# Kernel tuning notes

Hardware: AMD Instinct MI355X
Metric: run time of the kernel (lower is better)

## Reference

```python
import jax, jax.numpy as jnp
import numpy as np

B, N, E = 1, 100000, 1250000
IN, OUT = 128, 64


def setup_inputs() -> dict:
    key = jax.random.key(0)
    k = jax.random.split(key, 5)
    x = jax.random.normal(k[0], (B, N, IN), jnp.float32)
    edge_index = jax.random.randint(k[1], (B, 2, E), 0, N, dtype=jnp.int32)
    rank_mapping = jnp.zeros((2, E), jnp.int32)  # single-rank: all zeros
    W1 = jax.random.normal(k[2], (IN, OUT), jnp.float32) / np.sqrt(IN)
    Wp = jax.random.normal(k[3], (2 * OUT, 1), jnp.float32) / np.sqrt(2 * OUT)
    bp = jnp.zeros((1,), jnp.float32)
    bias = jnp.zeros((OUT,), jnp.float32)
    return {"x": x, "edge_index": edge_index, "rank_mapping": rank_mapping,
            "W1": W1, "Wp": Wp, "bp": bp, "bias": bias}


def reference(x, edge_index, rank_mapping, W1, Wp, bp, bias):
    # x: [B, N, IN]; edge_index: [B, 2, E]
    del rank_mapping  # comm routing metadata; identity on a single rank
    n = x.shape[1]
    h = jnp.einsum('bnf,fo->bno', x, W1)          # conv1 (no bias)
    src = edge_index[:, 0, :]                     # [B, E]
    dst = edge_index[:, 1, :]
    h_i = jnp.take_along_axis(h, dst[..., None], axis=1)   # gather at dst
    h_j = jnp.take_along_axis(h, src[..., None], axis=1)   # gather at src
    messages = jnp.concatenate([h_i, h_j], axis=-1)        # [B, E, 2*OUT]
    s = jnp.einsum('bec,co->beo', messages, Wp) + bp       # project_message
    s = jnp.where(s >= 0, s, 0.2 * s)                      # LeakyReLU(0.2)
    numerator = jnp.exp(s)                                 # [B, E, 1]
    seg = jax.vmap(lambda v, i: jax.ops.segment_sum(v, i, num_segments=n))
    denominator = seg(numerator, dst)                      # [B, N, 1]
    # NOTE: original gathers denominator with the *src* indices — replicated.
    denom_e = jnp.take_along_axis(denominator, src[..., None], axis=1)
    alpha = numerator / (denom_e + 1e-16)                  # [B, E, 1]
    out = seg(h_j * alpha, dst)                            # scatter-aggregate
    return out + bias
```

## Files before the change

### kernel.cpp

```cpp
#include <hip/hip_runtime.h>


#define MAXB 1024
#define EPB 4096
#define BIN_CAP 2560

typedef __attribute__((ext_vector_type(8))) short short8v;
typedef __attribute__((ext_vector_type(4))) float floatx4;

static __device__ __forceinline__ float bf2f(unsigned short u) {
    unsigned v = (unsigned)u << 16;
    return __builtin_bit_cast(float, v);
}
static __device__ __forceinline__ unsigned short f2bf(float f) {
    unsigned u = __builtin_bit_cast(unsigned, f);
    u = (u + 0x7FFFu + ((u >> 16) & 1u)) >> 16;
    return (unsigned short)u;
}

__global__ __launch_bounds__(256) void fused_nt_count_kernel(
    const float* __restrict__ x, const float* __restrict__ W1,
    const float* __restrict__ Wp, const int* __restrict__ ei,
    unsigned short* __restrict__ hbD, float* __restrict__ aArr,
    float* __restrict__ bArr, int* __restrict__ C, int N, int E, int G8, int B)
{
    __shared__ __align__(16) unsigned short w1b[4][4][4][16][8];
    __shared__ int cnt[MAXB];
    const int tid = threadIdx.x;

    if (blockIdx.x < G8) {
        const int g = blockIdx.x;
        for (int i = tid; i < B; i += 256) cnt[i] = 0;
        __syncthreads();
        const int base = g * EPB;
        #pragma unroll
        for (int k = 0; k < EPB / 256; ++k) {
            int e = base + k * 256 + tid;
            if (e < E) atomicAdd(&cnt[ei[E + e] >> 7], 1);
        }
        __syncthreads();
        for (int i = tid; i < B; i += 256) C[(size_t)g * B + i] = cnt[i];
        return;
    }

    for (int i = tid; i < 128 * 64; i += 256) {
        int k = i >> 6, o = i & 63;
        w1b[k >> 5][o >> 4][(k >> 3) & 3][o & 15][k & 7] = f2bf(W1[i]);
    }

    const int w = tid >> 6, lane = tid & 63;
    const int hi = lane >> 4, col = lane & 15;
    float wpa4[4], wpb4[4];
    #pragma unroll
    for (int ot = 0; ot < 4; ++ot) {
        wpa4[ot] = Wp[ot * 16 + col];
        wpb4[ot] = Wp[64 + ot * 16 + col];
    }
    __syncthreads();

    const int grp0 = (blockIdx.x - G8) * 4;
    #pragma unroll
    for (int gi = 0; gi < 4; ++gi) {
        const int gbase = (grp0 + gi) * 64;
        if (gbase >= N) break;
        const int n0 = gbase + w * 16;
        int arow = n0 + col; if (arow >= N) arow = N - 1;
        const float* xrow = x + (size_t)arow * 128 + hi * 8;

        floatx4 acc[4] = {{0.f,0.f,0.f,0.f},{0.f,0.f,0.f,0.f},
                          {0.f,0.f,0.f,0.f},{0.f,0.f,0.f,0.f}};
        #pragma unroll
        for (int kb = 0; kb < 4; ++kb) {
            float4 x0 = *reinterpret_cast<const float4*>(xrow + kb * 32);
            float4 x1 = *reinterpret_cast<const float4*>(xrow + kb * 32 + 4);
            short8v af;
            af[0] = (short)f2bf(x0.x); af[1] = (short)f2bf(x0.y);
            af[2] = (short)f2bf(x0.z); af[3] = (short)f2bf(x0.w);
            af[4] = (short)f2bf(x1.x); af[5] = (short)f2bf(x1.y);
            af[6] = (short)f2bf(x1.z); af[7] = (short)f2bf(x1.w);
            #pragma unroll
            for (int ot = 0; ot < 4; ++ot) {
                short8v bf = *reinterpret_cast<const short8v*>(&w1b[kb][ot][hi][col][0]);
                acc[ot] = __builtin_amdgcn_mfma_f32_16x16x32_bf16(af, bf, acc[ot], 0, 0, 0);
            }
        }

        #pragma unroll
        for (int ot = 0; ot < 4; ++ot) {
            #pragma unroll
            for (int r = 0; r < 4; ++r) {
                int n = n0 + hi * 4 + r;
                if (n < N) hbD[(size_t)n * 64 + ot * 16 + col] = f2bf(acc[ot][r]);
            }
        }
        #pragma unroll
        for (int r = 0; r < 4; ++r) {
            float pa = acc[0][r] * wpa4[0] + acc[1][r] * wpa4[1]
                     + acc[2][r] * wpa4[2] + acc[3][r] * wpa4[3];
            float pb = acc[0][r] * wpb4[0] + acc[1][r] * wpb4[1]
                     + acc[2][r] * wpb4[2] + acc[3][r] * wpb4[3];
            #pragma unroll
            for (int m = 1; m <= 8; m <<= 1) {
                pa += __shfl_xor(pa, m);
                pb += __shfl_xor(pb, m);
            }
            int n = n0 + hi * 4 + r;
            if (col == r && n < N) { aArr[n] = pa; bArr[n] = pb; }
        }
    }
}

__global__ __launch_bounds__(256) void colscan_kernel(
    int* __restrict__ C, int* __restrict__ S, int G8, int B)
{
    __shared__ int s[256];
    const int b = blockIdx.x, t = threadIdx.x;
    const int gp = G8 >> 3;
    int i0 = 2 * t, i1 = 2 * t + 1;
    int ga = 8 * (i0 % gp) + (i0 / gp);
    int gb = 8 * (i1 % gp) + (i1 / gp);
    int c0 = (i0 < G8) ? C[(size_t)ga * B + b] : 0;
    int c1 = (i1 < G8) ? C[(size_t)gb * B + b] : 0;
    int v = c0 + c1;
    s[t] = v;
    __syncthreads();
    for (int off = 1; off < 256; off <<= 1) {
        int u = (t >= off) ? s[t - off] : 0;
        __syncthreads();
        s[t] += u;
        __syncthreads();
    }
    int ex = s[t] - v;
    if (i0 < G8) C[(size_t)ga * B + b] = ex;
    if (i1 < G8) C[(size_t)gb * B + b] = ex + c0;
    if (t == 255) S[b] = s[255];
}

__global__ __launch_bounds__(256) void binscan_kernel(
    const int* __restrict__ S, int* __restrict__ binStart,
    int* __restrict__ offsets, int B, int N, int E)
{
    __shared__ int ts[256];
    const int t = threadIdx.x;
    const int chunk = (B + 255) >> 8;
    const int base = t * chunk, lim = min(B, base + chunk);
    int s = 0;
    for (int i = base; i < lim; ++i) s += S[i];
    ts[t] = s;
    __syncthreads();
    for (int off = 1; off < 256; off <<= 1) {
        int u = (t >= off) ? ts[t - off] : 0;
        __syncthreads();
        ts[t] += u;
        __syncthreads();
    }
    int run = ts[t] - s;
    for (int i = base; i < lim; ++i) { binStart[i] = run; run += S[i]; }
    if (t == 0) { binStart[B] = E; offsets[N] = E; }
}

__global__ __launch_bounds__(1024) void pass2_kernel(
    const int* __restrict__ ei, const float* __restrict__ aArr,
    const float* __restrict__ bArr, const float* __restrict__ bp,
    const int* __restrict__ C, const int* __restrict__ binStart,
    int2* __restrict__ staging, int E, int B)
{
    __shared__ int cur[MAXB];
    const int g = blockIdx.x, t = threadIdx.x;
    for (int i = t; i < B; i += 1024)
        cur[i] = binStart[i] + C[(size_t)g * B + i];
    __syncthreads();
    const float bp0 = bp[0];
    const int base = g * EPB;
    #pragma unroll
    for (int k = 0; k < EPB / 1024; ++k) {
        int e = base + k * 1024 + t;
        if (e >= E) break;
        int src = ei[e];
        int dst = ei[E + e];
        float s = aArr[dst] + bArr[src] + bp0;
        s = (s >= 0.f) ? s : 0.2f * s;
        float num = __expf(s);
        int bin = dst >> 7;
        int pos = atomicAdd(&cur[bin], 1);
        staging[pos] = make_int2(((dst & 127) << 17) | src, __float_as_int(num));
    }
}

__global__ __launch_bounds__(256) void localsort_kernel(
    const int* __restrict__ binStart, int2* __restrict__ staging,
    int* __restrict__ offsets, float* __restrict__ invD, int N)
{
    __shared__ int2 sEnt[BIN_CAP];
    __shared__ int sCnt[256], sScan[256], sCur[128];
    __shared__ float dsum[128];
    const int b = blockIdx.x, t = threadIdx.x;
    const int sBeg = binStart[b];
    const int count = min(binStart[b + 1] - sBeg, BIN_CAP);

    sCnt[t] = 0;
    if (t < 128) { sCur[t] = 0; dsum[t] = 0.f; }
    __syncthreads();
    for (int i = t; i < count; i += 256) {
        int2 e = staging[sBeg + i];
        sEnt[i] = e;
        int dl = e.x >> 17;
        atomicAdd(&sCnt[dl], 1);
        atomicAdd(&dsum[dl], __int_as_float(e.y));
    }
    __syncthreads();
    const int n0 = b << 7;
    const int Cl = min(128, N - n0);
    if (t < Cl) invD[n0 + t] = 1.f / (dsum[t] + 1e-16f);
    int v = sCnt[t];
    sScan[t] = v;
    __syncthreads();
    for (int off = 1; off < 256; off <<= 1) {
        int u = (t >= off) ? sScan[t - off] : 0;
        __syncthreads();
        sScan[t] += u;
        __syncthreads();
    }
    int ex = sScan[t] - v;
    __syncthreads();
    sScan[t] = ex;
    if (t < Cl) offsets[n0 + t] = sBeg + ex;
    __syncthreads();
    for (int i = t; i < count; i += 256) {
        int2 e = sEnt[i];
        int dl = e.x >> 17;
        int pos = sBeg + sScan[dl] + atomicAdd(&sCur[dl], 1);
        staging[pos] = make_int2(e.x & 0x1FFFF, e.y);
    }
}

__global__ __launch_bounds__(256) void aggregate_kernel(
    const int* __restrict__ offsets, const int2* __restrict__ sortedPair,
    const uint2* __restrict__ hbQ, const float* __restrict__ invD,
    const float* __restrict__ bias, float* __restrict__ out, int N)
{
    int gw = (blockIdx.x * blockDim.x + threadIdx.x) >> 6;
    int lane = threadIdx.x & 63;
    if (gw >= N) return;
    int beg = offsets[gw], end = offsets[gw + 1];
    const int quarter = lane >> 4;
    const int cg = lane & 15;
    float a0 = 0.f, a1 = 0.f, a2 = 0.f, a3 = 0.f;
    for (int e0 = beg; e0 < end; e0 += 64) {
        int idx = e0 + lane;
        int srcL = 0; float wL = 0.f;
        if (idx < end) {
            int2 p = sortedPair[idx];
            srcL = p.x;
            wL = __int_as_float(p.y) * invD[p.x];
        }
        int cnt = min(64, end - e0);
        int j = 0;
        for (; j + 16 <= cnt; j += 16) {
            #pragma unroll
            for (int u = 0; u < 4; ++u) {
                int jj = j + 4 * u + quarter;
                int s = __shfl(srcL, jj);
                float wv = __shfl(wL, jj);
                uint2 g = hbQ[(size_t)s * 16 + cg];
                a0 = fmaf(bf2f((unsigned short)(g.x & 0xFFFFu)), wv, a0);
                a1 = fmaf(bf2f((unsigned short)(g.x >> 16)), wv, a1);
                a2 = fmaf(bf2f((unsigned short)(g.y & 0xFFFFu)), wv, a2);
                a3 = fmaf(bf2f((unsigned short)(g.y >> 16)), wv, a3);
            }
        }
        for (; j < cnt; j += 4) {
            int jj = j + quarter;
            int s = __shfl(srcL, jj);
            float wv = __shfl(wL, jj);
            uint2 g = hbQ[(size_t)s * 16 + cg];
            a0 = fmaf(bf2f((unsigned short)(g.x & 0xFFFFu)), wv, a0);
            a1 = fmaf(bf2f((unsigned short)(g.x >> 16)), wv, a1);
            a2 = fmaf(bf2f((unsigned short)(g.y & 0xFFFFu)), wv, a2);
            a3 = fmaf(bf2f((unsigned short)(g.y >> 16)), wv, a3);
        }
    }
    a0 += __shfl_xor(a0, 16); a0 += __shfl_xor(a0, 32);
    a1 += __shfl_xor(a1, 16); a1 += __shfl_xor(a1, 32);
    a2 += __shfl_xor(a2, 16); a2 += __shfl_xor(a2, 32);
    a3 += __shfl_xor(a3, 16); a3 += __shfl_xor(a3, 32);
    if (lane < 16) {
        float4 bq = reinterpret_cast<const float4*>(bias)[cg];
        float4 o;
        o.x = a0 + bq.x; o.y = a1 + bq.y; o.z = a2 + bq.z; o.w = a3 + bq.w;
        reinterpret_cast<float4*>(out)[(size_t)gw * 16 + cg] = o;
    }
}

extern "C" void kernel_launch(void* const* d_in, const int* in_sizes, int n_in,
                              void* d_out, int out_size, void* d_ws, size_t ws_size,
                              hipStream_t stream) {
    const float* x    = (const float*)d_in[0];
    const int*   ei   = (const int*)d_in[1];
    const float* W1   = (const float*)d_in[3];
    const float* Wp   = (const float*)d_in[4];
    const float* bp   = (const float*)d_in[5];
    const float* bias = (const float*)d_in[6];
    float* out = (float*)d_out;

    const int N = in_sizes[0] / 128;
    const int E = in_sizes[1] / 2;
    const int B = (N + 127) >> 7;
    const int G = (E + EPB - 1) / EPB;
    const int G8 = (G + 7) & ~7;
    const int NTB = (N + 255) / 256;

    unsigned short* hbD = (unsigned short*)d_ws;
    float* aArr     = (float*)(hbD + (size_t)N * 64);
    float* bArr     = aArr + N;
    float* invD     = bArr + N;
    int*   C        = (int*)(invD + N);
    int*   S        = C + (size_t)G8 * B;
    int*   binStart = S + B;
    int*   offsets  = binStart + (B + 1);
    int*   stRaw    = offsets + (N + 1);
    stRaw = (int*)(((uintptr_t)stRaw + 7) & ~(uintptr_t)7);
    int2*  staging  = (int2*)stRaw;

    fused_nt_count_kernel<<<G8 + NTB, 256, 0, stream>>>(
        x, W1, Wp, ei, hbD, aArr, bArr, C, N, E, G8, B);

    colscan_kernel<<<B, 256, 0, stream>>>(C, S, G8, B);

    binscan_kernel<<<1, 256, 0, stream>>>(S, binStart, offsets, B, N, E);

    pass2_kernel<<<G8, 1024, 0, stream>>>(ei, aArr, bArr, bp, C, binStart,
                                          staging, E, B);

    localsort_kernel<<<B, 256, 0, stream>>>(binStart, staging, offsets, invD, N);

    aggregate_kernel<<<(N * 64 + 255) / 256, 256, 0, stream>>>(
        offsets, staging, reinterpret_cast<const uint2*>(hbD), invD, bias, out, N);
}
```

Baseline: 118.7 us.

## Accumulate softmax denominator with global atomics and prenormalize edge weights in localsort

Moves the per-destination denominator sum out of the localsort shared-memory reduction and into global float atomics in pass2, using a zeroed denom buffer. Localsort now divides each edge's numerator by denom[src] and stores the final weight, so aggregate no longer gathers invD per edge. The cost is 1.25M global atomics plus an extra memset launch. Atomic float ordering makes the sums nondeterministic.

```diff
diff --git a/kernel.cpp b/kernel.cpp
--- a/kernel.cpp
+++ b/kernel.cpp
@@ -163,7 +163,7 @@
     const int* __restrict__ ei, const float* __restrict__ aArr,
     const float* __restrict__ bArr, const float* __restrict__ bp,
     const int* __restrict__ C, const int* __restrict__ binStart,
-    int2* __restrict__ staging, int E, int B)
+    int2* __restrict__ staging, float* __restrict__ denom, int E, int B)
 {
     __shared__ int cur[MAXB];
     const int g = blockIdx.x, t = threadIdx.x;
@@ -181,6 +181,7 @@
         float s = aArr[dst] + bArr[src] + bp0;
         s = (s >= 0.f) ? s : 0.2f * s;
         float num = __expf(s);
+        atomicAdd(&denom[dst], num);
         int bin = dst >> 7;
         int pos = atomicAdd(&cur[bin], 1);
         staging[pos] = make_int2(((dst & 127) << 17) | src, __float_as_int(num));
@@ -189,55 +190,53 @@
 
 __global__ __launch_bounds__(256) void localsort_kernel(
     const int* __restrict__ binStart, int2* __restrict__ staging,
-    int* __restrict__ offsets, float* __restrict__ invD, int N)
+    int* __restrict__ offsets, const float* __restrict__ denom, int N)
 {
     __shared__ int2 sEnt[BIN_CAP];
     __shared__ int sCnt[256], sScan[256], sCur[128];
-    __shared__ float dsum[128];
     const int b = blockIdx.x, t = threadIdx.x;
     const int sBeg = binStart[b];
     const int count = min(binStart[b + 1] - sBeg, BIN_CAP);
 
     sCnt[t] = 0;
-    if (t < 128) { sCur[t] = 0; dsum[t] = 0.f; }
+    if (t < 128) sCur[t] = 0;
     __syncthreads();
     for (int i = t; i < count; i += 256) {
         int2 e = staging[sBeg + i];
         sEnt[i] = e;
-        int dl = e.x >> 17;
-        atomicAdd(&sCnt[dl], 1);
-        atomicAdd(&dsum[dl], __int_as_float(e.y));
-    }
-    __syncthreads();
+        atomicAdd(&sCnt[e.x >> 17], 1);
+    }
+    __syncthreads();
+    int v = sCnt[t];
+    sScan[t] = v;
+    __syncthreads();
+    for (int off = 1; off < 256; off <<= 1) {
+        int u = (t >= off) ? sScan[t - off] : 0;
+        __syncthreads();
+        sScan[t] += u;
+        __syncthreads();
+    }
+    int ex = sScan[t] - v;
+    __syncthreads();
+    sScan[t] = ex;
     const int n0 = b << 7;
     const int Cl = min(128, N - n0);
-    if (t < Cl) invD[n0 + t] = 1.f / (dsum[t] + 1e-16f);
-    int v = sCnt[t];
-    sScan[t] = v;
-    __syncthreads();
-    for (int off = 1; off < 256; off <<= 1) {
-        int u = (t >= off) ? sScan[t - off] : 0;
-        __syncthreads();
-        sScan[t] += u;
-        __syncthreads();
-    }
-    int ex = sScan[t] - v;
-    __syncthreads();
-    sScan[t] = ex;
     if (t < Cl) offsets[n0 + t] = sBeg + ex;
     __syncthreads();
     for (int i = t; i < count; i += 256) {
         int2 e = sEnt[i];
         int dl = e.x >> 17;
+        int src = e.x & 0x1FFFF;
+        float wgt = __int_as_float(e.y) / (denom[src] + 1e-16f);
         int pos = sBeg + sScan[dl] + atomicAdd(&sCur[dl], 1);
-        staging[pos] = make_int2(e.x & 0x1FFFF, e.y);
+        staging[pos] = make_int2(src, __float_as_int(wgt));
     }
 }
 
 __global__ __launch_bounds__(256) void aggregate_kernel(
     const int* __restrict__ offsets, const int2* __restrict__ sortedPair,
-    const uint2* __restrict__ hbQ, const float* __restrict__ invD,
-    const float* __restrict__ bias, float* __restrict__ out, int N)
+    const uint2* __restrict__ hbQ, const float* __restrict__ bias,
+    float* __restrict__ out, int N)
 {
     int gw = (blockIdx.x * blockDim.x + threadIdx.x) >> 6;
     int lane = threadIdx.x & 63;
@@ -252,7 +251,7 @@
         if (idx < end) {
             int2 p = sortedPair[idx];
             srcL = p.x;
-            wL = __int_as_float(p.y) * invD[p.x];
+            wL = __int_as_float(p.y);
         }
         int cnt = min(64, end - e0);
         int j = 0;
@@ -313,8 +312,8 @@
     unsigned short* hbD = (unsigned short*)d_ws;
     float* aArr     = (float*)(hbD + (size_t)N * 64);
     float* bArr     = aArr + N;
-    float* invD     = bArr + N;
-    int*   C        = (int*)(invD + N);
+    float* denom    = bArr + N;
+    int*   C        = (int*)(denom + N);
     int*   S        = C + (size_t)G8 * B;
     int*   binStart = S + B;
     int*   offsets  = binStart + (B + 1);
@@ -322,6 +321,8 @@
     stRaw = (int*)(((uintptr_t)stRaw + 7) & ~(uintptr_t)7);
     int2*  staging  = (int2*)stRaw;
 
+    hipMemsetAsync(denom, 0, (size_t)N * sizeof(float), stream);
+
     fused_nt_count_kernel<<<G8 + NTB, 256, 0, stream>>>(
         x, W1, Wp, ei, hbD, aArr, bArr, C, N, E, G8, B);
 
@@ -330,10 +331,10 @@
     binscan_kernel<<<1, 256, 0, stream>>>(S, binStart, offsets, B, N, E);
 
     pass2_kernel<<<G8, 1024, 0, stream>>>(ei, aArr, bArr, bp, C, binStart,
-                                          staging, E, B);
-
-    localsort_kernel<<<B, 256, 0, stream>>>(binStart, staging, offsets, invD, N);
+                                          staging, denom, E, B);
+
+    localsort_kernel<<<B, 256, 0, stream>>>(binStart, staging, offsets, denom, N);
 
     aggregate_kernel<<<(N * 64 + 255) / 256, 256, 0, stream>>>(
-        offsets, staging, reinterpret_cast<const uint2*>(hbD), invD, bias, out, N);
-}
+        offsets, staging, reinterpret_cast<const uint2*>(hbD), bias, out, N);
+}
```

New measurement: 172.2 us. 45.0% more time.
